# Kernel optimization log

Hardware: AMD Instinct MI355X
Metric: run time of the kernel (lower is better)

## Reference

```python
import jax, jax.numpy as jnp
import numpy as np

N = 4096      # nodes
IN = 512      # in_features
HEADS = 8
HPH = 8       # n_hidden // n_heads
HID = HEADS * HPH  # 64
CLS = 16      # n_classes
NEG_SLOPE = 0.2
MASK_VAL = -1e9


def setup_inputs() -> dict:
    key = jax.random.key(0)
    ks = jax.random.split(key, 8)
    x = jax.random.normal(ks[0], (N, IN), jnp.float32)
    # sparse-ish adjacency, avg degree ~16, with self loops
    adj = jax.random.bernoulli(ks[1], 16.0 / N, (N, N)) | jnp.eye(N, dtype=bool)
    W1 = jax.random.normal(ks[2], (IN, HEADS, HPH), jnp.float32) * 0.05
    a1l = jax.random.normal(ks[3], (HEADS, HPH), jnp.float32) * 0.05
    a1r = jax.random.normal(ks[4], (HEADS, HPH), jnp.float32) * 0.05
    W2 = jax.random.normal(ks[5], (HID, 1, CLS), jnp.float32) * 0.05
    a2l = jax.random.normal(ks[6], (1, CLS), jnp.float32) * 0.05
    a2r = jax.random.normal(ks[7], (1, CLS), jnp.float32) * 0.05
    return {"x": x, "adj": adj, "W1": W1, "a1l": a1l, "a1r": a1r,
            "W2": W2, "a2l": a2l, "a2r": a2r}


def gat_layer(x, adj, W, al, ar, is_concat):
    # project: [N, H, D]
    g = jnp.einsum('ni,ihd->nhd', x, W)
    # score e[i,j,h] = leaky_relu(a_l . g_i + a_r . g_j)
    sl = jnp.einsum('nhd,hd->nh', g, al)  # [N, H]
    sr = jnp.einsum('nhd,hd->nh', g, ar)  # [N, H]
    e = jax.nn.leaky_relu(sl[:, None, :] + sr[None, :, :], NEG_SLOPE)  # [N, N, H]
    e = jnp.where(adj[:, :, None], e, MASK_VAL)
    a = jax.nn.softmax(e, axis=1)                 # softmax over neighbors j
    out = jnp.einsum('ijh,jhd->ihd', a, g)        # [N, H, D]
    if is_concat:
        return out.reshape(out.shape[0], -1)      # [N, H*D]
    return out.mean(axis=1)                        # [N, D]


def reference(x, adj, W1, a1l, a1r, W2, a2l, a2r):
    # dropout layers are identity in eval mode
    h = gat_layer(x, adj, W1, a1l, a1r, True)   # [N, HID]
    h = jax.nn.elu(h)
    return gat_layer(h, adj, W2, a2l, a2r, False)  # [N, CLS]
```

## Files before the change

### kernel.cpp

```cpp
#include <hip/hip_runtime.h>
#include <hip/hip_bf16.h>

#define N_NODES 4096
#define IN_F 512
#define HEADS 8
#define HPH 8
#define HID 64
#define CLS 16
#define NEG_SLOPE 0.2f
#define MAXD 256

__device__ __forceinline__ float leaky(float x) { return x > 0.f ? x : NEG_SLOPE * x; }

__global__ __launch_bounds__(256, 2) void scan_proj1(
        const int* __restrict__ adj,
        const float* __restrict__ x,
        const float* __restrict__ W1,
        const float* __restrict__ a1l,
        const float* __restrict__ a1r,
        float* __restrict__ g1,
        float* __restrict__ sl1,
        float* __restrict__ sr1,
        int* __restrict__ deg_g,
        int* __restrict__ nbr_g) {
    __shared__ float xs[4][516];
    const int b = blockIdx.x;
    const int t = threadIdx.x;
    if (b < N_NODES / 4) {
        int* nbrS = (int*)&xs[0][0];
        __shared__ int cntS[4];
        const int w = t >> 6, lane = t & 63;
        if (lane == 0) cntS[w] = 0;
        const int i = b * 4 + w;
        const int4* row = (const int4*)(adj + (size_t)i * N_NODES);
        int4 v[16];
#pragma unroll
        for (int s = 0; s < 16; ++s) v[s] = row[lane + 64 * s];
#pragma unroll
        for (int s = 0; s < 16; ++s) {
            const int base = 4 * (lane + 64 * s);
            if (v[s].x | v[s].y | v[s].z | v[s].w) {
                if (v[s].x) { int p = atomicAdd(&cntS[w], 1); if (p < MAXD) nbrS[w * MAXD + p] = base; }
                if (v[s].y) { int p = atomicAdd(&cntS[w], 1); if (p < MAXD) nbrS[w * MAXD + p] = base + 1; }
                if (v[s].z) { int p = atomicAdd(&cntS[w], 1); if (p < MAXD) nbrS[w * MAXD + p] = base + 2; }
                if (v[s].w) { int p = atomicAdd(&cntS[w], 1); if (p < MAXD) nbrS[w * MAXD + p] = base + 3; }
            }
        }
        const int n = cntS[w] < MAXD ? cntS[w] : MAXD;
        if (lane == 0) deg_g[i] = n;
        for (int k = lane; k < n; k += 64) nbr_g[(size_t)i * MAXD + k] = nbrS[w * MAXD + k];
        return;
    }
    const int i0 = (b - N_NODES / 4) * 4;
    const int nl = t >> 6;
    const int inner = t & 63;
    const int kq = inner >> 4;
    const int cg = inner & 15;
    for (int l = t; l < 512; l += 256) {
        const int r = l >> 7, c4 = l & 127;
        *(float4*)&xs[r][c4 * 4] = *(const float4*)(x + (size_t)(i0 + r) * IN_F + c4 * 4);
    }
    __syncthreads();
    float4 acc = make_float4(0.f, 0.f, 0.f, 0.f);
    const float* xrow = &xs[nl][kq * 128];
    const float* Wq = W1 + (size_t)(kq * 128) * HID + cg * 4;
#pragma unroll 4
    for (int k = 0; k < 128; k += 4) {
        const float4 xv = *(const float4*)(xrow + k);
        const float4 w0 = *(const float4*)(Wq + (size_t)(k + 0) * HID);
        const float4 w1 = *(const float4*)(Wq + (size_t)(k + 1) * HID);
        const float4 w2 = *(const float4*)(Wq + (size_t)(k + 2) * HID);
        const float4 w3 = *(const float4*)(Wq + (size_t)(k + 3) * HID);
        acc.x += xv.x * w0.x + xv.y * w1.x + xv.z * w2.x + xv.w * w3.x;
        acc.y += xv.x * w0.y + xv.y * w1.y + xv.z * w2.y + xv.w * w3.y;
        acc.z += xv.x * w0.z + xv.y * w1.z + xv.z * w2.z + xv.w * w3.z;
        acc.w += xv.x * w0.w + xv.y * w1.w + xv.z * w2.w + xv.w * w3.w;
    }
#pragma unroll
    for (int m = 16; m <= 32; m <<= 1) {
        acc.x += __shfl_xor(acc.x, m, 64);
        acc.y += __shfl_xor(acc.y, m, 64);
        acc.z += __shfl_xor(acc.z, m, 64);
        acc.w += __shfl_xor(acc.w, m, 64);
    }
    if (kq == 0) {
        const int i = i0 + nl;
        *(float4*)(g1 + (size_t)i * HID + cg * 4) = acc;
        const float4 al = *(const float4*)(a1l + cg * 4);
        const float4 ar = *(const float4*)(a1r + cg * 4);
        float pl = acc.x * al.x + acc.y * al.y + acc.z * al.z + acc.w * al.w;
        float pr = acc.x * ar.x + acc.y * ar.y + acc.z * ar.z + acc.w * ar.w;
        pl += __shfl_xor(pl, 1, 64);
        pr += __shfl_xor(pr, 1, 64);
        if ((cg & 1) == 0) {
            sl1[i * HEADS + (cg >> 1)] = pl;
            sr1[i * HEADS + (cg >> 1)] = pr;
        }
    }
}

__global__ __launch_bounds__(64) void attn1_fused(
        const float* __restrict__ g1,
        const float* __restrict__ sl1,
        const float* __restrict__ sr1,
        const float* __restrict__ W2,
        const float* __restrict__ a2l,
        const float* __restrict__ a2r,
        const int* __restrict__ deg_g,
        const int* __restrict__ nbr_g,
        float* __restrict__ g2,
        float* __restrict__ sl2,
        float* __restrict__ sr2) {
    const int i = blockIdx.x;
    const int t = threadIdx.x;
    __shared__ int nbr[MAXD];
    __shared__ float h1s[HID];
    const int n = deg_g[i];
    for (int k = t; k < n; k += 64) nbr[k] = nbr_g[(size_t)i * MAXD + k];
    __syncthreads();
    const int h = t >> 3;
    const float sl = sl1[i * HEADS + h];
    float denom = 0.f, acc = 0.f;
    int k = 0;
    for (; k + 4 <= n; k += 4) {
        const int j0 = nbr[k], j1 = nbr[k + 1], j2 = nbr[k + 2], j3 = nbr[k + 3];
        const float s0 = sr1[j0 * HEADS + h], s1 = sr1[j1 * HEADS + h];
        const float s2 = sr1[j2 * HEADS + h], s3 = sr1[j3 * HEADS + h];
        const float v0 = g1[(size_t)j0 * HID + t], v1 = g1[(size_t)j1 * HID + t];
        const float v2 = g1[(size_t)j2 * HID + t], v3 = g1[(size_t)j3 * HID + t];
        const float w0 = __expf(leaky(sl + s0)), w1 = __expf(leaky(sl + s1));
        const float w2 = __expf(leaky(sl + s2)), w3 = __expf(leaky(sl + s3));
        denom += (w0 + w1) + (w2 + w3);
        acc += w0 * v0; acc += w1 * v1; acc += w2 * v2; acc += w3 * v3;
    }
    for (; k < n; ++k) {
        const int jj = nbr[k];
        const float w = __expf(leaky(sl + sr1[jj * HEADS + h]));
        denom += w;
        acc += w * g1[(size_t)jj * HID + t];
    }
    float o = (n > 0) ? (acc / denom) : 0.f;
    o = (o > 0.f) ? o : expm1f(o);
    h1s[t] = o;
    __syncthreads();
    const int q = t >> 4, c = t & 15;
    float p = 0.f;
#pragma unroll
    for (int kk = 0; kk < 16; ++kk) {
        const int k2 = q * 16 + kk;
        p += h1s[k2] * W2[k2 * CLS + c];
    }
    p += __shfl_xor(p, 16, 64);
    p += __shfl_xor(p, 32, 64);
    float pl = 0.f, pr = 0.f;
    if (t < CLS) {
        g2[(size_t)i * CLS + t] = p;
        pl = p * a2l[t];
        pr = p * a2r[t];
    }
#pragma unroll
    for (int off = 1; off < 16; off <<= 1) {
        pl += __shfl_xor(pl, off, 64);
        pr += __shfl_xor(pr, off, 64);
    }
    if (t == 0) { sl2[i] = pl; sr2[i] = pr; }
}

__global__ __launch_bounds__(64) void attn2(
        const int* __restrict__ deg_g,
        const int* __restrict__ nbr_g,
        const float* __restrict__ g2,
        const float* __restrict__ sl2,
        const float* __restrict__ sr2,
        float* __restrict__ out) {
    const int t = threadIdx.x;
    const int g = t >> 4;
    const int c = t & 15;
    const int node = blockIdx.x * 4 + g;
    __shared__ int nbrs[4][MAXD];
    const int n = deg_g[node];
    for (int k = c; k < n; k += 16) nbrs[g][k] = nbr_g[(size_t)node * MAXD + k];
    __syncthreads();
    const float sl = sl2[node];
    float denom = 0.f, acc = 0.f;
    int k = 0;
    for (; k + 4 <= n; k += 4) {
        const int j0 = nbrs[g][k], j1 = nbrs[g][k + 1];
        const int j2 = nbrs[g][k + 2], j3 = nbrs[g][k + 3];
        const float s0 = sr2[j0], s1 = sr2[j1], s2 = sr2[j2], s3 = sr2[j3];
        const float v0 = g2[(size_t)j0 * CLS + c], v1 = g2[(size_t)j1 * CLS + c];
        const float v2 = g2[(size_t)j2 * CLS + c], v3 = g2[(size_t)j3 * CLS + c];
        const float w0 = __expf(leaky(sl + s0)), w1 = __expf(leaky(sl + s1));
        const float w2 = __expf(leaky(sl + s2)), w3 = __expf(leaky(sl + s3));
        denom += (w0 + w1) + (w2 + w3);
        acc += w0 * v0; acc += w1 * v1; acc += w2 * v2; acc += w3 * v3;
    }
    for (; k < n; ++k) {
        const int jj = nbrs[g][k];
        const float w = __expf(leaky(sl + sr2[jj]));
        denom += w;
        acc += w * g2[(size_t)jj * CLS + c];
    }
    out[(size_t)node * CLS + c] = (n > 0) ? acc / denom : 0.f;
}

extern "C" void kernel_launch(void* const* d_in, const int* in_sizes, int n_in,
                              void* d_out, int out_size, void* d_ws, size_t ws_size,
                              hipStream_t stream) {
    const float* x   = (const float*)d_in[0];
    const int*   adj = (const int*)d_in[1];
    const float* W1  = (const float*)d_in[2];
    const float* a1l = (const float*)d_in[3];
    const float* a1r = (const float*)d_in[4];
    const float* W2  = (const float*)d_in[5];
    const float* a2l = (const float*)d_in[6];
    const float* a2r = (const float*)d_in[7];
    float* out = (float*)d_out;

    float* ws  = (float*)d_ws;
    float* g1  = ws;
    float* sl1 = g1  + (size_t)N_NODES * HID;
    float* sr1 = sl1 + (size_t)N_NODES * HEADS;
    float* g2  = sr1 + (size_t)N_NODES * HEADS;
    float* sl2 = g2  + (size_t)N_NODES * CLS;
    float* sr2 = sl2 + N_NODES;
    int*   deg = (int*)(sr2 + N_NODES);
    int*   nbr = deg + N_NODES;

    scan_proj1<<<2 * (N_NODES / 4), 256, 0, stream>>>(
        adj, x, W1, a1l, a1r, g1, sl1, sr1, deg, nbr);
    attn1_fused<<<N_NODES, 64, 0, stream>>>(g1, sl1, sr1, W2, a2l, a2r,
                                            deg, nbr, g2, sl2, sr2);
    attn2<<<N_NODES / 4, 64, 0, stream>>>(deg, nbr, g2, sl2, sr2, out);
}
```

Before: 136.4 us.

## Interleave adjacency-scan and projection blocks, tile projection over 16 rows, pack attention blocks

scan_proj1 now arranges blocks in groups of five: four blocks scan adjacency rows and one projects 16 rows of x. Each projection wave keeps four row accumulators so every W1 load is reused four times, and the projection work runs alongside the bandwidth-heavy adjacency scan instead of in a separate tail. attn1 and attn2 now pack 4 and 16 nodes into 256-thread blocks, with one wave-private shared buffer per node, and drop __syncthreads. Leaving out the barrier assumes lockstep execution within a wave for LDS visibility, and the four-row register tile raises register pressure.

```diff
diff --git a/kernel.cpp b/kernel.cpp
--- a/kernel.cpp
+++ b/kernel.cpp
@@ -12,7 +12,7 @@
 
 __device__ __forceinline__ float leaky(float x) { return x > 0.f ? x : NEG_SLOPE * x; }
 
-__global__ __launch_bounds__(256, 2) void scan_proj1(
+__global__ __launch_bounds__(256, 4) void scan_proj1(
         const int* __restrict__ adj,
         const float* __restrict__ x,
         const float* __restrict__ W1,
@@ -23,15 +23,17 @@
         float* __restrict__ sr1,
         int* __restrict__ deg_g,
         int* __restrict__ nbr_g) {
-    __shared__ float xs[4][516];
+    __shared__ float xs[16][516];
+    __shared__ int cntS[4];
     const int b = blockIdx.x;
     const int t = threadIdx.x;
-    if (b < N_NODES / 4) {
+    const int group = b / 5;
+    const int role = b - group * 5;
+    if (role < 4) {
         int* nbrS = (int*)&xs[0][0];
-        __shared__ int cntS[4];
         const int w = t >> 6, lane = t & 63;
         if (lane == 0) cntS[w] = 0;
-        const int i = b * 4 + w;
+        const int i = (group * 4 + role) * 4 + w;
         const int4* row = (const int4*)(adj + (size_t)i * N_NODES);
         int4 v[16];
 #pragma unroll
@@ -51,55 +53,68 @@
         for (int k = lane; k < n; k += 64) nbr_g[(size_t)i * MAXD + k] = nbrS[w * MAXD + k];
         return;
     }
-    const int i0 = (b - N_NODES / 4) * 4;
-    const int nl = t >> 6;
+    const int i0 = group * 16;
+    for (int l = t; l < 2048; l += 256) {
+        const int r = l >> 7, c4 = l & 127;
+        *(float4*)&xs[r][c4 * 4] = *(const float4*)(x + (size_t)(i0 + r) * IN_F + c4 * 4);
+    }
+    __syncthreads();
+    const int wv = t >> 6;
     const int inner = t & 63;
     const int kq = inner >> 4;
     const int cg = inner & 15;
-    for (int l = t; l < 512; l += 256) {
-        const int r = l >> 7, c4 = l & 127;
-        *(float4*)&xs[r][c4 * 4] = *(const float4*)(x + (size_t)(i0 + r) * IN_F + c4 * 4);
-    }
-    __syncthreads();
-    float4 acc = make_float4(0.f, 0.f, 0.f, 0.f);
-    const float* xrow = &xs[nl][kq * 128];
+    float4 acc[4];
+#pragma unroll
+    for (int r = 0; r < 4; ++r) acc[r] = make_float4(0.f, 0.f, 0.f, 0.f);
+    const float* xr[4];
+#pragma unroll
+    for (int r = 0; r < 4; ++r) xr[r] = &xs[wv * 4 + r][kq * 128];
     const float* Wq = W1 + (size_t)(kq * 128) * HID + cg * 4;
-#pragma unroll 4
+#pragma unroll 2
     for (int k = 0; k < 128; k += 4) {
-        const float4 xv = *(const float4*)(xrow + k);
         const float4 w0 = *(const float4*)(Wq + (size_t)(k + 0) * HID);
         const float4 w1 = *(const float4*)(Wq + (size_t)(k + 1) * HID);
         const float4 w2 = *(const float4*)(Wq + (size_t)(k + 2) * HID);
         const float4 w3 = *(const float4*)(Wq + (size_t)(k + 3) * HID);
-        acc.x += xv.x * w0.x + xv.y * w1.x + xv.z * w2.x + xv.w * w3.x;
-        acc.y += xv.x * w0.y + xv.y * w1.y + xv.z * w2.y + xv.w * w3.y;
-        acc.z += xv.x * w0.z + xv.y * w1.z + xv.z * w2.z + xv.w * w3.z;
-        acc.w += xv.x * w0.w + xv.y * w1.w + xv.z * w2.w + xv.w * w3.w;
-    }
-#pragma unroll
-    for (int m = 16; m <= 32; m <<= 1) {
-        acc.x += __shfl_xor(acc.x, m, 64);
-        acc.y += __shfl_xor(acc.y, m, 64);
-        acc.z += __shfl_xor(acc.z, m, 64);
-        acc.w += __shfl_xor(acc.w, m, 64);
+#pragma unroll
+        for (int r = 0; r < 4; ++r) {
+            const float4 xv = *(const float4*)(xr[r] + k);
+            acc[r].x += xv.x * w0.x + xv.y * w1.x + xv.z * w2.x + xv.w * w3.x;
+            acc[r].y += xv.x * w0.y + xv.y * w1.y + xv.z * w2.y + xv.w * w3.y;
+            acc[r].z += xv.x * w0.z + xv.y * w1.z + xv.z * w2.z + xv.w * w3.z;
+            acc[r].w += xv.x * w0.w + xv.y * w1.w + xv.z * w2.w + xv.w * w3.w;
+        }
+    }
+#pragma unroll
+    for (int r = 0; r < 4; ++r) {
+#pragma unroll
+        for (int m = 16; m <= 32; m <<= 1) {
+            acc[r].x += __shfl_xor(acc[r].x, m, 64);
+            acc[r].y += __shfl_xor(acc[r].y, m, 64);
+            acc[r].z += __shfl_xor(acc[r].z, m, 64);
+            acc[r].w += __shfl_xor(acc[r].w, m, 64);
+        }
     }
     if (kq == 0) {
-        const int i = i0 + nl;
-        *(float4*)(g1 + (size_t)i * HID + cg * 4) = acc;
         const float4 al = *(const float4*)(a1l + cg * 4);
         const float4 ar = *(const float4*)(a1r + cg * 4);
-        float pl = acc.x * al.x + acc.y * al.y + acc.z * al.z + acc.w * al.w;
-        float pr = acc.x * ar.x + acc.y * ar.y + acc.z * ar.z + acc.w * ar.w;
-        pl += __shfl_xor(pl, 1, 64);
-        pr += __shfl_xor(pr, 1, 64);
-        if ((cg & 1) == 0) {
-            sl1[i * HEADS + (cg >> 1)] = pl;
-            sr1[i * HEADS + (cg >> 1)] = pr;
-        }
-    }
-}
-
-__global__ __launch_bounds__(64) void attn1_fused(
+#pragma unroll
+        for (int r = 0; r < 4; ++r) {
+            const int i = i0 + wv * 4 + r;
+            *(float4*)(g1 + (size_t)i * HID + cg * 4) = acc[r];
+            float pl = acc[r].x * al.x + acc[r].y * al.y + acc[r].z * al.z + acc[r].w * al.w;
+            float pr = acc[r].x * ar.x + acc[r].y * ar.y + acc[r].z * ar.z + acc[r].w * ar.w;
+            pl += __shfl_xor(pl, 1, 64);
+            pr += __shfl_xor(pr, 1, 64);
+            if ((cg & 1) == 0) {
+                sl1[i * HEADS + (cg >> 1)] = pl;
+                sr1[i * HEADS + (cg >> 1)] = pr;
+            }
+        }
+    }
+}
+
+__global__ __launch_bounds__(256) void attn1_fused(
         const float* __restrict__ g1,
         const float* __restrict__ sl1,
         const float* __restrict__ sr1,
@@ -111,19 +126,19 @@
         float* __restrict__ g2,
         float* __restrict__ sl2,
         float* __restrict__ sr2) {
-    const int i = blockIdx.x;
-    const int t = threadIdx.x;
-    __shared__ int nbr[MAXD];
-    __shared__ float h1s[HID];
+    __shared__ int nbr[4][MAXD];
+    __shared__ float h1s[4][HID];
+    const int w = threadIdx.x >> 6;
+    const int t = threadIdx.x & 63;
+    const int i = blockIdx.x * 4 + w;
     const int n = deg_g[i];
-    for (int k = t; k < n; k += 64) nbr[k] = nbr_g[(size_t)i * MAXD + k];
-    __syncthreads();
+    for (int k = t; k < n; k += 64) nbr[w][k] = nbr_g[(size_t)i * MAXD + k];
     const int h = t >> 3;
     const float sl = sl1[i * HEADS + h];
     float denom = 0.f, acc = 0.f;
     int k = 0;
     for (; k + 4 <= n; k += 4) {
-        const int j0 = nbr[k], j1 = nbr[k + 1], j2 = nbr[k + 2], j3 = nbr[k + 3];
+        const int j0 = nbr[w][k], j1 = nbr[w][k + 1], j2 = nbr[w][k + 2], j3 = nbr[w][k + 3];
         const float s0 = sr1[j0 * HEADS + h], s1 = sr1[j1 * HEADS + h];
         const float s2 = sr1[j2 * HEADS + h], s3 = sr1[j3 * HEADS + h];
         const float v0 = g1[(size_t)j0 * HID + t], v1 = g1[(size_t)j1 * HID + t];
@@ -134,21 +149,20 @@
         acc += w0 * v0; acc += w1 * v1; acc += w2 * v2; acc += w3 * v3;
     }
     for (; k < n; ++k) {
-        const int jj = nbr[k];
-        const float w = __expf(leaky(sl + sr1[jj * HEADS + h]));
-        denom += w;
-        acc += w * g1[(size_t)jj * HID + t];
+        const int jj = nbr[w][k];
+        const float wq = __expf(leaky(sl + sr1[jj * HEADS + h]));
+        denom += wq;
+        acc += wq * g1[(size_t)jj * HID + t];
     }
     float o = (n > 0) ? (acc / denom) : 0.f;
     o = (o > 0.f) ? o : expm1f(o);
-    h1s[t] = o;
-    __syncthreads();
+    h1s[w][t] = o;
     const int q = t >> 4, c = t & 15;
     float p = 0.f;
 #pragma unroll
     for (int kk = 0; kk < 16; ++kk) {
         const int k2 = q * 16 + kk;
-        p += h1s[k2] * W2[k2 * CLS + c];
+        p += h1s[w][k2] * W2[k2 * CLS + c];
     }
     p += __shfl_xor(p, 16, 64);
     p += __shfl_xor(p, 32, 64);
@@ -166,27 +180,28 @@
     if (t == 0) { sl2[i] = pl; sr2[i] = pr; }
 }
 
-__global__ __launch_bounds__(64) void attn2(
+__global__ __launch_bounds__(256) void attn2(
         const int* __restrict__ deg_g,
         const int* __restrict__ nbr_g,
         const float* __restrict__ g2,
         const float* __restrict__ sl2,
         const float* __restrict__ sr2,
         float* __restrict__ out) {
-    const int t = threadIdx.x;
+    __shared__ int nbrs[16][MAXD];
+    const int w = threadIdx.x >> 6;
+    const int t = threadIdx.x & 63;
     const int g = t >> 4;
     const int c = t & 15;
-    const int node = blockIdx.x * 4 + g;
-    __shared__ int nbrs[4][MAXD];
+    const int node = blockIdx.x * 16 + w * 4 + g;
+    int* myn = nbrs[w * 4 + g];
     const int n = deg_g[node];
-    for (int k = c; k < n; k += 16) nbrs[g][k] = nbr_g[(size_t)node * MAXD + k];
-    __syncthreads();
+    for (int k = c; k < n; k += 16) myn[k] = nbr_g[(size_t)node * MAXD + k];
     const float sl = sl2[node];
     float denom = 0.f, acc = 0.f;
     int k = 0;
     for (; k + 4 <= n; k += 4) {
-        const int j0 = nbrs[g][k], j1 = nbrs[g][k + 1];
-        const int j2 = nbrs[g][k + 2], j3 = nbrs[g][k + 3];
+        const int j0 = myn[k], j1 = myn[k + 1];
+        const int j2 = myn[k + 2], j3 = myn[k + 3];
         const float s0 = sr2[j0], s1 = sr2[j1], s2 = sr2[j2], s3 = sr2[j3];
         const float v0 = g2[(size_t)j0 * CLS + c], v1 = g2[(size_t)j1 * CLS + c];
         const float v2 = g2[(size_t)j2 * CLS + c], v3 = g2[(size_t)j3 * CLS + c];
@@ -196,10 +211,10 @@
         acc += w0 * v0; acc += w1 * v1; acc += w2 * v2; acc += w3 * v3;
     }
     for (; k < n; ++k) {
-        const int jj = nbrs[g][k];
-        const float w = __expf(leaky(sl + sr2[jj]));
-        denom += w;
-        acc += w * g2[(size_t)jj * CLS + c];
+        const int jj = myn[k];
+        const float wq = __expf(leaky(sl + sr2[jj]));
+        denom += wq;
+        acc += wq * g2[(size_t)jj * CLS + c];
     }
     out[(size_t)node * CLS + c] = (n > 0) ? acc / denom : 0.f;
 }
@@ -227,9 +242,9 @@
     int*   deg = (int*)(sr2 + N_NODES);
     int*   nbr = deg + N_NODES;
 
-    scan_proj1<<<2 * (N_NODES / 4), 256, 0, stream>>>(
+    scan_proj1<<<5 * (N_NODES / 16), 256, 0, stream>>>(
         adj, x, W1, a1l, a1r, g1, sl1, sr1, deg, nbr);
-    attn1_fused<<<N_NODES, 64, 0, stream>>>(g1, sl1, sr1, W2, a2l, a2r,
-                                            deg, nbr, g2, sl2, sr2);
-    attn2<<<N_NODES / 4, 64, 0, stream>>>(deg, nbr, g2, sl2, sr2, out);
-}
+    attn1_fused<<<N_NODES / 4, 256, 0, stream>>>(g1, sl1, sr1, W2, a2l, a2r,
+                                                 deg, nbr, g2, sl2, sr2);
+    attn2<<<N_NODES / 16, 256, 0, stream>>>(deg, nbr, g2, sl2, sr2, out);
+}
```

Result: faster. 129.1 us (-5.3%).
